# Kernel tuning notes

Measured on AMD Instinct MI355X. Metric: run time of the kernel, lower is better.

Reference implementation:

```python
import jax, jax.numpy as jnp
import numpy as np

B, T = 64, 1024
VOCAB, EMBED, HIDDEN = 55, 64, 128


def setup_inputs() -> dict:
    key = jax.random.key(0)
    ks = jax.random.split(key, 15)
    stdv = 1.0 / np.sqrt(HIDDEN)
    u = lambda k, s: jax.random.uniform(k, s, jnp.float32, -stdv, stdv)
    return {
        "x": jax.random.randint(ks[0], (B, T), 0, VOCAB),
        "emb": jax.random.normal(ks[1], (VOCAB, EMBED), jnp.float32),
        "w_ih0": u(ks[2], (HIDDEN, EMBED)),
        "b_ih0": u(ks[3], (HIDDEN,)),
        "w_hh0": u(ks[4], (HIDDEN, HIDDEN)),
        "b_hh0": u(ks[5], (HIDDEN,)),
        "w_ih1": u(ks[6], (HIDDEN, HIDDEN)),
        "b_ih1": u(ks[7], (HIDDEN,)),
        "w_hh1": u(ks[8], (HIDDEN, HIDDEN)),
        "b_hh1": u(ks[9], (HIDDEN,)),
        "attn_w": u(ks[10], (HIDDEN, HIDDEN)),
        "attn_b": u(ks[11], (HIDDEN,)),
        "fc_w": u(ks[12], (VOCAB, 2 * HIDDEN)),
        "fc_b": u(ks[13], (VOCAB,)),
    }


def reference(x, emb, w_ih0, b_ih0, w_hh0, b_hh0, w_ih1, b_ih1, w_hh1, b_hh1,
              attn_w, attn_b, fc_w, fc_b):
    Bx, Tx = x.shape
    H = w_hh0.shape[0]
    e = emb[x]  # [B, T, E]

    def step(carry, x_t):  # x_t: [B, E]
        h0, h1 = carry
        h0 = jnp.tanh(x_t @ w_ih0.T + b_ih0 + h0 @ w_hh0.T + b_hh0)
        h1 = jnp.tanh(h0 @ w_ih1.T + b_ih1 + h1 @ w_hh1.T + b_hh1)
        return (h0, h1), h1

    init = (jnp.zeros((Bx, H), e.dtype), jnp.zeros((Bx, H), e.dtype))
    _, outs = jax.lax.scan(step, init, jnp.swapaxes(e, 0, 1))  # [T, B, H]
    outs = jnp.swapaxes(outs, 0, 1)  # [B, T, H]

    Q = outs @ attn_w.T + attn_b  # [B, T, H]
    scores = jnp.einsum('bth,bsh->bts', Q, outs) / jnp.sqrt(jnp.asarray(H, e.dtype))
    causal = jnp.tril(jnp.ones((Tx, Tx), bool))  # [T, T]
    scores = jnp.where(causal[None], scores, jnp.asarray(-jnp.inf, scores.dtype))
    attn = jax.nn.softmax(scores, axis=-1)
    context = jnp.einsum('bts,bsh->bth', attn, outs)  # [B, T, H]

    combined = jnp.concatenate([outs, context], axis=-1)  # [B, T, 2H]
    logits = combined @ fc_w.T + fc_b  # [B, T, vocab]
    return logits
```

## Files before the change

### kernel.cpp

```cpp
#include <hip/hip_runtime.h>
#include <hip/hip_bf16.h>
#include <cstdint>
#include <cstddef>


typedef __attribute__((ext_vector_type(8))) short short8;
typedef __attribute__((ext_vector_type(4))) float f32x4;

__device__ __forceinline__ float bf2f(unsigned short u) {
    union { unsigned int i; float f; } c; c.i = ((unsigned int)u) << 16; return c.f;
}
__device__ __forceinline__ unsigned short f2bf(float f) {
    union { float f; unsigned int i; } c; c.f = f;
    unsigned int u = c.i;
    u += 0x7fffu + ((u >> 16) & 1u);
    return (unsigned short)(u >> 16);
}
__device__ __forceinline__ unsigned int pk_bf16(float lo, float hi) {
    union { __hip_bfloat162 h2; unsigned int u; } c;
    c.h2 = __float22bfloat162_rn(make_float2(lo, hi));
    return c.u;
}
__device__ __forceinline__ float fast_tanh(float x) {
    float e = __expf(2.0f * x);
    return 1.0f - 2.0f * __builtin_amdgcn_rcpf(e + 1.0f);
}
__device__ __forceinline__ void bar_lds() {
    asm volatile("s_waitcnt lgkmcnt(0)\n\ts_barrier" ::: "memory");
}
__device__ __forceinline__ short8 ld_a_bf16(const float* p) {
    const float4* q = (const float4*)p;
    float4 f0 = q[0], f1 = q[1];
    short8 r;
    r[0]=(short)f2bf(f0.x); r[1]=(short)f2bf(f0.y);
    r[2]=(short)f2bf(f0.z); r[3]=(short)f2bf(f0.w);
    r[4]=(short)f2bf(f1.x); r[5]=(short)f2bf(f1.y);
    r[6]=(short)f2bf(f1.z); r[7]=(short)f2bf(f1.w);
    return r;
}
__device__ __forceinline__ void ld_fc_hilo(const float* p, short8& hi, short8& lo) {
    const float4* q = (const float4*)p;
    float4 f0 = q[0], f1 = q[1];
    float ff[8] = {f0.x, f0.y, f0.z, f0.w, f1.x, f1.y, f1.z, f1.w};
#pragma unroll
    for (int i = 0; i < 8; ++i) {
        unsigned short hb = f2bf(ff[i]);
        hi[i] = (short)hb;
        lo[i] = (short)f2bf(ff[i] - bf2f(hb));
    }
}

__global__ __launch_bounds__(128)
void k_we(const float* __restrict__ emb, const float* __restrict__ w_ih0,
          const float* __restrict__ b_ih0, const float* __restrict__ b_hh0,
          float* __restrict__ WE)
{
    __shared__ float ev[64];
    const int i = threadIdx.x;
    const int v = blockIdx.x;
    if (i < 64) ev[i] = emb[v * 64 + i];
    __syncthreads();
    float s = b_ih0[i] + b_hh0[i];
    const float* wr = w_ih0 + i * 64;
#pragma unroll
    for (int k = 0; k < 64; ++k) s += wr[k] * ev[k];
    WE[v * 128 + i] = s;
}

__global__ __launch_bounds__(256)
void k_weg(const int* __restrict__ x, const float* __restrict__ WE,
           float* __restrict__ WEg)
{
    __shared__ int xv[32];
    const int tid = threadIdx.x;
    const int b   = blockIdx.y;
    const int t0  = blockIdx.x * 32;
    if (tid < 32) xv[tid] = x[b * 1024 + t0 + tid];
    __syncthreads();
#pragma unroll
    for (int it = 0; it < 4; ++it) {
        int tt = it * 8 + (tid >> 5);
        int c4 = tid & 31;
        float4 v = ((const float4*)(WE + xv[tt] * 128))[c4];
        ((float4*)(WEg + ((size_t)b * 1024 + t0 + tt) * 128))[c4] = v;
    }
}

#define A_STEP(T, P, E0, E1)                                                   \
  {                                                                            \
    const unsigned short* h0p = &h0buf[P][n][quad * 8];                        \
    short8 bh[4];                                                              \
    _Pragma("unroll")                                                          \
    for (int ks = 0; ks < 4; ++ks)                                             \
      bh[ks] = *(const short8*)(h0p + ks * 32);                                \
    f32x4 c0 = (f32x4){E0.x, E0.y, E0.z, E0.w};                                \
    f32x4 c1 = (f32x4){E1.x, E1.y, E1.z, E1.w};                                \
    {                                                                          \
      const size_t tp = (size_t)(((T) + 3 < 1024) ? (T) + 3 : 1023) * 128;     \
      E0 = *(const float4*)(WEg + wegB0 + tp);                                 \
      E1 = *(const float4*)(WEg + wegB1 + tp);                                 \
    }                                                                          \
    _Pragma("unroll")                                                          \
    for (int ks = 0; ks < 4; ++ks) {                                           \
      c0 = __builtin_amdgcn_mfma_f32_16x16x32_bf16(a0[0][ks], bh[ks], c0, 0, 0, 0); \
      c1 = __builtin_amdgcn_mfma_f32_16x16x32_bf16(a0[1][ks], bh[ks], c1, 0, 0, 0); \
    }                                                                          \
    *(uint2*)&h0buf[(P) ^ 1][n][r0] = make_uint2(                              \
        pk_bf16(fast_tanh(c0[0]), fast_tanh(c0[1])),                           \
        pk_bf16(fast_tanh(c0[2]), fast_tanh(c0[3])));                          \
    *(uint2*)&h0buf[(P) ^ 1][n][r1] = make_uint2(                              \
        pk_bf16(fast_tanh(c1[0]), fast_tanh(c1[1])),                           \
        pk_bf16(fast_tanh(c1[2]), fast_tanh(c1[3])));                          \
    bar_lds();                                                                 \
  }

#define B_STEP(T, P)                                                           \
  {                                                                            \
    const unsigned short* h0p = &h0buf[P][n][quad * 8];                        \
    const unsigned short* h1p = &h1buf[P][n][quad * 8];                        \
    short8 bh0[4], bh1[4];                                                     \
    _Pragma("unroll")                                                          \
    for (int ks = 0; ks < 4; ++ks) {                                           \
      bh0[ks] = *(const short8*)(h0p + ks * 32);                               \
      bh1[ks] = *(const short8*)(h1p + ks * 32);                               \
    }                                                                          \
    f32x4 c0 = b1i[0], c1 = b1i[1];                                            \
    f32x4 d0 = (f32x4){0.f, 0.f, 0.f, 0.f};                                    \
    f32x4 d1 = (f32x4){0.f, 0.f, 0.f, 0.f};                                    \
    _Pragma("unroll")                                                          \
    for (int ks = 0; ks < 4; ++ks) {                                           \
      c0 = __builtin_amdgcn_mfma_f32_16x16x32_bf16(a1[0][ks], bh0[ks], c0, 0, 0, 0); \
      c1 = __builtin_amdgcn_mfma_f32_16x16x32_bf16(a1[1][ks], bh0[ks], c1, 0, 0, 0); \
      d0 = __builtin_amdgcn_mfma_f32_16x16x32_bf16(a2[0][ks], bh1[ks], d0, 0, 0, 0); \
      d1 = __builtin_amdgcn_mfma_f32_16x16x32_bf16(a2[1][ks], bh1[ks], d1, 0, 0, 0); \
    }                                                                          \
    uint2 o0 = make_uint2(                                                     \
        pk_bf16(fast_tanh(c0[0] + d0[0]), fast_tanh(c0[1] + d0[1])),           \
        pk_bf16(fast_tanh(c0[2] + d0[2]), fast_tanh(c0[3] + d0[3])));          \
    uint2 o1 = make_uint2(                                                     \
        pk_bf16(fast_tanh(c1[0] + d1[0]), fast_tanh(c1[1] + d1[1])),           \
        pk_bf16(fast_tanh(c1[2] + d1[2]), fast_tanh(c1[3] + d1[3])));          \
    *(uint2*)&h1buf[(P) ^ 1][n][r0] = o0;                                      \
    *(uint2*)&h1buf[(P) ^ 1][n][r1] = o1;                                      \
    *(uint2*)(outp0 + (size_t)(T) * 128) = o0;                                 \
    *(uint2*)(outp1 + (size_t)(T) * 128) = o1;                                 \
    bar_lds();                                                                 \
  }

__global__ __launch_bounds__(512, 1)
void k_scan7(const float* __restrict__ WEg,
             const float* __restrict__ w_hh0,
             const float* __restrict__ w_ih1, const float* __restrict__ b_ih1,
             const float* __restrict__ w_hh1, const float* __restrict__ b_hh1,
             unsigned short* __restrict__ outs_bf)
{
    const int tid   = threadIdx.x;
    const int w     = tid >> 6;
    const int lane  = tid & 63;
    const int quad  = lane >> 4;
    const int n     = lane & 15;
    const int bbase = blockIdx.x * 16;

    __shared__ __align__(16) unsigned short h0buf[2][16][136];
    __shared__ __align__(16) unsigned short h1buf[2][16][136];

    if (w < 4) {
        const int r0 = w * 32 + quad * 4;
        const int r1 = r0 + 16;
        short8 a0[2][4];
#pragma unroll
        for (int r = 0; r < 2; ++r) {
            const size_t mrow = (size_t)(w * 32 + r * 16 + n) * 128;
#pragma unroll
            for (int ks = 0; ks < 4; ++ks)
                a0[r][ks] = ld_a_bf16(w_hh0 + mrow + ks * 32 + quad * 8);
        }
        const size_t wegB0 = (size_t)(bbase + n) * 131072 + r0;
        const size_t wegB1 = wegB0 + 16;
        {
            float4 p0 = *(const float4*)(WEg + wegB0);
            float4 p1 = *(const float4*)(WEg + wegB1);
            *(uint2*)&h0buf[0][n][r0] = make_uint2(
                pk_bf16(fast_tanh(p0.x), fast_tanh(p0.y)),
                pk_bf16(fast_tanh(p0.z), fast_tanh(p0.w)));
            *(uint2*)&h0buf[0][n][r1] = make_uint2(
                pk_bf16(fast_tanh(p1.x), fast_tanh(p1.y)),
                pk_bf16(fast_tanh(p1.z), fast_tanh(p1.w)));
        }
        float4 eA0 = *(const float4*)(WEg + wegB0 + 128);
        float4 eA1 = *(const float4*)(WEg + wegB1 + 128);
        float4 eB0 = *(const float4*)(WEg + wegB0 + 256);
        float4 eB1 = *(const float4*)(WEg + wegB1 + 256);
        __syncthreads();

        for (int t = 0; t < 1022; t += 2) {
            A_STEP(t,     0, eA0, eA1);
            A_STEP(t + 1, 1, eB0, eB1);
        }
        A_STEP(1022, 0, eA0, eA1);
        bar_lds();
    } else {
        const int w2 = w - 4;
        const int r0 = w2 * 32 + quad * 4;
        const int r1 = r0 + 16;
        short8 a1[2][4], a2[2][4];
#pragma unroll
        for (int r = 0; r < 2; ++r) {
            const size_t mrow = (size_t)(w2 * 32 + r * 16 + n) * 128;
#pragma unroll
            for (int ks = 0; ks < 4; ++ks) {
                a1[r][ks] = ld_a_bf16(w_ih1 + mrow + ks * 32 + quad * 8);
                a2[r][ks] = ld_a_bf16(w_hh1 + mrow + ks * 32 + quad * 8);
            }
        }
        f32x4 b1i[2];
#pragma unroll
        for (int r = 0; r < 2; ++r)
#pragma unroll
            for (int j = 0; j < 4; ++j) {
                int row = w2 * 32 + r * 16 + quad * 4 + j;
                b1i[r][j] = b_ih1[row] + b_hh1[row];
            }
        *(uint2*)&h1buf[0][n][r0] = make_uint2(0u, 0u);
        *(uint2*)&h1buf[0][n][r1] = make_uint2(0u, 0u);
        unsigned short* outp0 = outs_bf + (size_t)(bbase + n) * 131072 + r0;
        unsigned short* outp1 = outp0 + 16;
        __syncthreads();

        for (int t = 0; t < 1022; t += 2) {
            B_STEP(t,     0);
            B_STEP(t + 1, 1);
        }
        B_STEP(1022, 0);
        B_STEP(1023, 1);
    }
}

__global__ __launch_bounds__(256)
void k_transpose(const unsigned short* __restrict__ outs_bf,
                 unsigned short* __restrict__ outsT)
{
    __shared__ unsigned short lt[128][130];
    const int tid = threadIdx.x;
    const int t0  = blockIdx.x * 128;
    const int b   = blockIdx.y;
    const unsigned int* src =
        (const unsigned int*)(outs_bf + ((size_t)b * 1024 + t0) * 128);
    for (int idx = tid; idx < 8192; idx += 256) {
        int tr = idx >> 6, h2 = idx & 63;
        unsigned int v = src[tr * 64 + h2];
        lt[tr][h2 * 2]     = (unsigned short)(v & 0xffffu);
        lt[tr][h2 * 2 + 1] = (unsigned short)(v >> 16);
    }
    __syncthreads();
    unsigned int* dst = (unsigned int*)(outsT + (size_t)b * 128 * 1024);
    for (int idx = tid; idx < 8192; idx += 256) {
        int h = idx >> 6, t2 = idx & 63;
        unsigned int v = (unsigned int)lt[t2 * 2][h] |
                         ((unsigned int)lt[t2 * 2 + 1][h] << 16);
        dst[h * 512 + (t0 >> 1) + t2] = v;
    }
}

__global__ __launch_bounds__(512, 1)
void k_attnfc(const unsigned short* __restrict__ outs_bf,
              const unsigned short* __restrict__ outsT,
              const float* __restrict__ attn_w, const float* __restrict__ attn_b,
              const float* __restrict__ fc_w, const float* __restrict__ fc_b,
              float* __restrict__ out)
{
    __shared__ __align__(16) unsigned char smem[100352];
    unsigned short* lK = (unsigned short*)smem;
    unsigned short* lV = (unsigned short*)(smem + 32768);
    unsigned short* lP = (unsigned short*)(smem + 65536);

    const int tid  = threadIdx.x;
    const int w    = tid >> 6;
    const int lane = tid & 63;
    const int quad = lane >> 4;
    const int n    = lane & 15;
    const int qt   = blockIdx.x;
    const int b    = blockIdx.y;
    unsigned short* lPw = lP + w * 2176;
    const float cscale = 0.08838834764831845f;

    const unsigned short* outsB = outs_bf + (size_t)b * 131072;
    const int qrow = qt * 128 + w * 16 + n;

    short8 bo[4];
#pragma unroll
    for (int ks = 0; ks < 4; ++ks)
        bo[ks] = *(const short8*)(outsB + (size_t)qrow * 128 + ks * 32 + quad * 8);
#pragma unroll
    for (int mt = 0; mt < 8; ++mt) {
        short8 aw[4];
#pragma unroll
        for (int ks = 0; ks < 4; ++ks)
            aw[ks] = ld_a_bf16(attn_w + (size_t)(mt * 16 + n) * 128 + ks * 32 + quad * 8);
        f32x4 cq;
#pragma unroll
        for (int r = 0; r < 4; ++r) cq[r] = attn_b[mt * 16 + quad * 4 + r];
#pragma unroll
        for (int ks = 0; ks < 4; ++ks)
            cq = __builtin_amdgcn_mfma_f32_16x16x32_bf16(aw[ks], bo[ks], cq, 0,0,0);
        *(uint2*)&lPw[n * 136 + mt * 16 + quad * 4] =
            make_uint2(pk_bf16(cq[0], cq[1]), pk_bf16(cq[2], cq[3]));
    }
    short8 qf[4];
#pragma unroll
    for (int ks = 0; ks < 4; ++ks)
        qf[ks] = *(const short8*)&lPw[n * 136 + ks * 32 + quad * 8];

    f32x4 accO[8];
#pragma unroll
    for (int dt = 0; dt < 8; ++dt) accO[dt] = (f32x4){0.f, 0.f, 0.f, 0.f};
    float mx = -1e30f, lsum = 0.f;

    for (int kt = 0; kt <= qt; ++kt) {
        __syncthreads();
        for (int c = tid; c < 2048; c += 512) {
            int row = c >> 4, k8 = c & 15;
            uint4 vk = *(const uint4*)(outsB + (size_t)(kt * 128 + row) * 128 + k8 * 8);
            *(uint4*)&lK[row * 128 + ((k8 ^ (row & 15)) << 3)] = vk;
            uint4 vv = *(const uint4*)(outsT + ((size_t)b * 128 + row) * 1024 +
                                       kt * 128 + k8 * 8);
            *(uint4*)&lV[row * 128 + ((k8 ^ (row & 15)) << 3)] = vv;
        }
        __syncthreads();
        f32x4 accS[8];
#pragma unroll
        for (int mt = 0; mt < 8; ++mt) {
            short8 af[4];
#pragma unroll
            for (int ks = 0; ks < 4; ++ks) {
                int r = mt * 16 + n;
                af[ks] = *(const short8*)&lK[r * 128 + (((ks * 4 + quad) ^ (r & 15)) << 3)];
            }
            f32x4 s = (f32x4){0.f, 0.f, 0.f, 0.f};
#pragma unroll
            for (int ks = 0; ks < 4; ++ks)
                s = __builtin_amdgcn_mfma_f32_16x16x32_bf16(af[ks], qf[ks], s, 0,0,0);
            accS[mt] = s;
        }
        if (kt == qt) {
            const int ql = w * 16 + n;
#pragma unroll
            for (int mt = 0; mt < 8; ++mt)
#pragma unroll
                for (int jv = 0; jv < 4; ++jv)
                    if (mt * 16 + quad * 4 + jv > ql) accS[mt][jv] = -1e30f;
        }
        float tmax = accS[0][0];
#pragma unroll
        for (int mt = 0; mt < 8; ++mt)
#pragma unroll
            for (int jv = 0; jv < 4; ++jv) tmax = fmaxf(tmax, accS[mt][jv]);
        tmax = fmaxf(tmax, __shfl_xor(tmax, 16));
        tmax = fmaxf(tmax, __shfl_xor(tmax, 32));
        float nm = fmaxf(mx, tmax);
        float alpha = __expf((mx - nm) * cscale);
        float ss = 0.f;
#pragma unroll
        for (int mt = 0; mt < 8; ++mt)
#pragma unroll
            for (int jv = 0; jv < 4; ++jv) {
                float p = __expf((accS[mt][jv] - nm) * cscale);
                accS[mt][jv] = p;
                ss += p;
            }
        ss += __shfl_xor(ss, 16);
        ss += __shfl_xor(ss, 32);
        lsum = lsum * alpha + ss;
        mx = nm;
#pragma unroll
        for (int mt = 0; mt < 8; ++mt)
            *(uint2*)&lPw[n * 136 + mt * 16 + quad * 4] = make_uint2(
                pk_bf16(accS[mt][0], accS[mt][1]),
                pk_bf16(accS[mt][2], accS[mt][3]));
#pragma unroll
        for (int dt = 0; dt < 8; ++dt)
#pragma unroll
            for (int jv = 0; jv < 4; ++jv) accO[dt][jv] *= alpha;
        short8 pf[4];
#pragma unroll
        for (int ks = 0; ks < 4; ++ks)
            pf[ks] = *(const short8*)&lPw[n * 136 + ks * 32 + quad * 8];
#pragma unroll
        for (int dt = 0; dt < 8; ++dt) {
            short8 vf[4];
#pragma unroll
            for (int ks = 0; ks < 4; ++ks) {
                int d = dt * 16 + n;
                vf[ks] = *(const short8*)&lV[d * 128 + (((ks * 4 + quad) ^ (d & 15)) << 3)];
            }
#pragma unroll
            for (int ks = 0; ks < 4; ++ks)
                accO[dt] = __builtin_amdgcn_mfma_f32_16x16x32_bf16(vf[ks], pf[ks], accO[dt], 0,0,0);
        }
    }
    {
        float inv = __builtin_amdgcn_rcpf(lsum);
#pragma unroll
        for (int dt = 0; dt < 8; ++dt)
            *(uint2*)&lPw[n * 136 + dt * 16 + quad * 4] = make_uint2(
                pk_bf16(accO[dt][0] * inv, accO[dt][1] * inv),
                pk_bf16(accO[dt][2] * inv, accO[dt][3] * inv));
    }
    short8 bC[4];
#pragma unroll
    for (int ks = 0; ks < 4; ++ks)
        bC[ks] = *(const short8*)&lPw[n * 136 + ks * 32 + quad * 8];
#pragma unroll
    for (int mt = 0; mt < 4; ++mt) {
        const int vrow = mt * 16 + n;
        f32x4 acc;
#pragma unroll
        for (int r = 0; r < 4; ++r) {
            int vv = mt * 16 + quad * 4 + r;
            acc[r] = (vv < 55) ? fc_b[vv] : 0.f;
        }
#pragma unroll
        for (int c = 0; c < 8; ++c) {
            short8 hi, lo;
            if (vrow < 55) {
                ld_fc_hilo(fc_w + (size_t)vrow * 256 + c * 32 + quad * 8, hi, lo);
            } else {
#pragma unroll
                for (int i = 0; i < 8; ++i) { hi[i] = 0; lo[i] = 0; }
            }
            short8 bb = (c < 4) ? bo[c] : bC[c - 4];
            acc = __builtin_amdgcn_mfma_f32_16x16x32_bf16(hi, bb, acc, 0,0,0);
            acc = __builtin_amdgcn_mfma_f32_16x16x32_bf16(lo, bb, acc, 0,0,0);
        }
#pragma unroll
        for (int r = 0; r < 4; ++r) {
            int vv = mt * 16 + quad * 4 + r;
            if (vv < 55)
                out[((size_t)b * 1024 + qrow) * 55 + vv] = acc[r];
        }
    }
}

extern "C" void kernel_launch(void* const* d_in, const int* in_sizes, int n_in,
                              void* d_out, int out_size, void* d_ws, size_t ws_size,
                              hipStream_t stream)
{
    const int*   x      = (const int*)d_in[0];
    const float* emb    = (const float*)d_in[1];
    const float* w_ih0  = (const float*)d_in[2];
    const float* b_ih0  = (const float*)d_in[3];
    const float* w_hh0  = (const float*)d_in[4];
    const float* b_hh0  = (const float*)d_in[5];
    const float* w_ih1  = (const float*)d_in[6];
    const float* b_ih1  = (const float*)d_in[7];
    const float* w_hh1  = (const float*)d_in[8];
    const float* b_hh1  = (const float*)d_in[9];
    const float* attn_w = (const float*)d_in[10];
    const float* attn_b = (const float*)d_in[11];
    const float* fc_w   = (const float*)d_in[12];
    const float* fc_b   = (const float*)d_in[13];
    float* out = (float*)d_out;

    char* ws = (char*)d_ws;
    unsigned short* outs_bf = (unsigned short*)(ws);
    unsigned short* outsT   = (unsigned short*)(ws + ((size_t)16 << 20));
    float*          WEp     = (float*)         (ws + ((size_t)32 << 20));
    float*          WEg     = (float*)         (ws + ((size_t)33 << 20));

    k_we<<<dim3(55), dim3(128), 0, stream>>>(emb, w_ih0, b_ih0, b_hh0, WEp);
    k_weg<<<dim3(32, 64), dim3(256), 0, stream>>>(x, WEp, WEg);
    k_scan7<<<dim3(4), dim3(512), 0, stream>>>(
        WEg, w_hh0, w_ih1, b_ih1, w_hh1, b_hh1, outs_bf);
    k_transpose<<<dim3(8, 64), dim3(256), 0, stream>>>(outs_bf, outsT);
    k_attnfc<<<dim3(8, 64), dim3(512), 0, stream>>>(
        outs_bf, outsT, attn_w, attn_b, fc_w, fc_b, out);
}
```

Before: 757.5 us.

## Shrink attention key tiles to 64 rows to cut LDS and causal waste

The flash-attention loop now streams K/V in 64-row tiles instead of 128, halving the LDS footprint to about 50KB. Finer tiles mean the diagonal query block skips more masked-out work, and the smaller LDS allocation could let more blocks share a CU. The cost is twice as many loop iterations and barriers, each with fewer MFMAs. The diff also leaves a dead no-op masking loop in place, and Q staging reuses the K buffer region, which needs an added barrier before the output write.

```diff
diff --git a/kernel.cpp b/kernel.cpp
--- a/kernel.cpp
+++ b/kernel.cpp
@@ -269,10 +269,10 @@
               const float* __restrict__ fc_w, const float* __restrict__ fc_b,
               float* __restrict__ out)
 {
-    __shared__ __align__(16) unsigned char smem[100352];
+    __shared__ __align__(16) unsigned char smem[51200];
     unsigned short* lK = (unsigned short*)smem;
-    unsigned short* lV = (unsigned short*)(smem + 32768);
-    unsigned short* lP = (unsigned short*)(smem + 65536);
+    unsigned short* lV = (unsigned short*)(smem + 16384);
+    unsigned short* lP = (unsigned short*)(smem + 32768);
 
     const int tid  = threadIdx.x;
     const int w    = tid >> 6;
@@ -281,7 +281,8 @@
     const int n    = lane & 15;
     const int qt   = blockIdx.x;
     const int b    = blockIdx.y;
-    unsigned short* lPw = lP + w * 2176;
+    unsigned short* lPw = lP + w * 1152;
+    unsigned short* lQw = ((unsigned short*)smem) + w * 2048;
     const float cscale = 0.08838834764831845f;
 
     const unsigned short* outsB = outs_bf + (size_t)b * 131072;
@@ -303,33 +304,39 @@
 #pragma unroll
         for (int ks = 0; ks < 4; ++ks)
             cq = __builtin_amdgcn_mfma_f32_16x16x32_bf16(aw[ks], bo[ks], cq, 0,0,0);
-        *(uint2*)&lPw[n * 136 + mt * 16 + quad * 4] =
+        *(uint2*)&lQw[n * 128 + mt * 16 + quad * 4] =
             make_uint2(pk_bf16(cq[0], cq[1]), pk_bf16(cq[2], cq[3]));
     }
     short8 qf[4];
 #pragma unroll
     for (int ks = 0; ks < 4; ++ks)
-        qf[ks] = *(const short8*)&lPw[n * 136 + ks * 32 + quad * 8];
+        qf[ks] = *(const short8*)&lQw[n * 128 + ks * 32 + quad * 8];
 
     f32x4 accO[8];
 #pragma unroll
     for (int dt = 0; dt < 8; ++dt) accO[dt] = (f32x4){0.f, 0.f, 0.f, 0.f};
     float mx = -1e30f, lsum = 0.f;
 
-    for (int kt = 0; kt <= qt; ++kt) {
+    const int ntiles = 2 * qt + 2;
+    for (int kt = 0; kt < ntiles; ++kt) {
         __syncthreads();
         for (int c = tid; c < 2048; c += 512) {
-            int row = c >> 4, k8 = c & 15;
-            uint4 vk = *(const uint4*)(outsB + (size_t)(kt * 128 + row) * 128 + k8 * 8);
-            *(uint4*)&lK[row * 128 + ((k8 ^ (row & 15)) << 3)] = vk;
-            uint4 vv = *(const uint4*)(outsT + ((size_t)b * 128 + row) * 1024 +
-                                       kt * 128 + k8 * 8);
-            *(uint4*)&lV[row * 128 + ((k8 ^ (row & 15)) << 3)] = vv;
+            if (c < 1024) {
+                int row = c >> 4, k8 = c & 15;
+                uint4 vk = *(const uint4*)(outsB + (size_t)(kt * 64 + row) * 128 + k8 * 8);
+                *(uint4*)&lK[row * 128 + ((k8 ^ (row & 15)) << 3)] = vk;
+            } else {
+                int c2 = c - 1024;
+                int d = c2 >> 3, t8 = c2 & 7;
+                uint4 vv = *(const uint4*)(outsT + ((size_t)b * 128 + d) * 1024 +
+                                           kt * 64 + t8 * 8);
+                *(uint4*)&lV[d * 64 + ((t8 ^ (d & 7)) << 3)] = vv;
+            }
         }
         __syncthreads();
-        f32x4 accS[8];
-#pragma unroll
-        for (int mt = 0; mt < 8; ++mt) {
+        f32x4 accS[4];
+#pragma unroll
+        for (int mt = 0; mt < 4; ++mt) {
             short8 af[4];
 #pragma unroll
             for (int ks = 0; ks < 4; ++ks) {
@@ -342,17 +349,27 @@
                 s = __builtin_amdgcn_mfma_f32_16x16x32_bf16(af[ks], qf[ks], s, 0,0,0);
             accS[mt] = s;
         }
-        if (kt == qt) {
+        if (kt >= 2 * qt) {
+#pragma unroll
+            for (int mt = 0; mt < 4; ++mt)
+#pragma unroll
+                for (int jv = 0; jv < 4; ++jv)
+                    if (kt * 64 + mt * 16 + quad * 4 + jv > qrow - qt * 128 + 0 + qt * 128 - qt * 128
+                        + qt * 128 - qt * 128 + (qrow & 127) - (qrow & 127) + (qrow - qt * 128))
+                        ;
+        }
+        if (kt >= 2 * qt) {
             const int ql = w * 16 + n;
 #pragma unroll
-            for (int mt = 0; mt < 8; ++mt)
+            for (int mt = 0; mt < 4; ++mt)
 #pragma unroll
                 for (int jv = 0; jv < 4; ++jv)
-                    if (mt * 16 + quad * 4 + jv > ql) accS[mt][jv] = -1e30f;
+                    if (kt * 64 + mt * 16 + quad * 4 + jv > qt * 128 + ql)
+                        accS[mt][jv] = -1e30f;
         }
         float tmax = accS[0][0];
 #pragma unroll
-        for (int mt = 0; mt < 8; ++mt)
+        for (int mt = 0; mt < 4; ++mt)
 #pragma unroll
             for (int jv = 0; jv < 4; ++jv) tmax = fmaxf(tmax, accS[mt][jv]);
         tmax = fmaxf(tmax, __shfl_xor(tmax, 16));
@@ -361,7 +378,7 @@
         float alpha = __expf((mx - nm) * cscale);
         float ss = 0.f;
 #pragma unroll
-        for (int mt = 0; mt < 8; ++mt)
+        for (int mt = 0; mt < 4; ++mt)
 #pragma unroll
             for (int jv = 0; jv < 4; ++jv) {
                 float p = __expf((accS[mt][jv] - nm) * cscale);
@@ -373,43 +390,44 @@
         lsum = lsum * alpha + ss;
         mx = nm;
 #pragma unroll
-        for (int mt = 0; mt < 8; ++mt)
-            *(uint2*)&lPw[n * 136 + mt * 16 + quad * 4] = make_uint2(
+        for (int mt = 0; mt < 4; ++mt)
+            *(uint2*)&lPw[n * 72 + mt * 16 + quad * 4] = make_uint2(
                 pk_bf16(accS[mt][0], accS[mt][1]),
                 pk_bf16(accS[mt][2], accS[mt][3]));
 #pragma unroll
         for (int dt = 0; dt < 8; ++dt)
 #pragma unroll
             for (int jv = 0; jv < 4; ++jv) accO[dt][jv] *= alpha;
-        short8 pf[4];
-#pragma unroll
-        for (int ks = 0; ks < 4; ++ks)
-            pf[ks] = *(const short8*)&lPw[n * 136 + ks * 32 + quad * 8];
+        short8 pf[2];
+#pragma unroll
+        for (int ks = 0; ks < 2; ++ks)
+            pf[ks] = *(const short8*)&lPw[n * 72 + ks * 32 + quad * 8];
 #pragma unroll
         for (int dt = 0; dt < 8; ++dt) {
-            short8 vf[4];
-#pragma unroll
-            for (int ks = 0; ks < 4; ++ks) {
+            short8 vf[2];
+#pragma unroll
+            for (int ks = 0; ks < 2; ++ks) {
                 int d = dt * 16 + n;
-                vf[ks] = *(const short8*)&lV[d * 128 + (((ks * 4 + quad) ^ (d & 15)) << 3)];
-            }
-#pragma unroll
-            for (int ks = 0; ks < 4; ++ks)
+                vf[ks] = *(const short8*)&lV[d * 64 + (((ks * 4 + quad) ^ (d & 7)) << 3)];
+            }
+#pragma unroll
+            for (int ks = 0; ks < 2; ++ks)
                 accO[dt] = __builtin_amdgcn_mfma_f32_16x16x32_bf16(vf[ks], pf[ks], accO[dt], 0,0,0);
         }
     }
+    __syncthreads();
     {
         float inv = __builtin_amdgcn_rcpf(lsum);
 #pragma unroll
         for (int dt = 0; dt < 8; ++dt)
-            *(uint2*)&lPw[n * 136 + dt * 16 + quad * 4] = make_uint2(
+            *(uint2*)&lQw[n * 128 + dt * 16 + quad * 4] = make_uint2(
                 pk_bf16(accO[dt][0] * inv, accO[dt][1] * inv),
                 pk_bf16(accO[dt][2] * inv, accO[dt][3] * inv));
     }
     short8 bC[4];
 #pragma unroll
     for (int ks = 0; ks < 4; ++ks)
-        bC[ks] = *(const short8*)&lPw[n * 136 + ks * 32 + quad * 8];
+        bC[ks] = *(const short8*)&lQw[n * 128 + ks * 32 + quad * 8];
 #pragma unroll
     for (int mt = 0; mt < 4; ++mt) {
         const int vrow = mt * 16 + n;
```

Result: faster. 742.6 us (-2.0%).
